# Optimization experiments

Measured on AMD Instinct MI355X. Metric: run time of the kernel, lower is better.

Reference implementation:

```python
import jax, jax.numpy as jnp
import numpy as np

N_NODES = 60000
IN_CH = 128
HID = 32
ACT_DIM = 6
N_EDGES = 600000


def setup_inputs() -> dict:
    key = jax.random.key(0)
    ks = jax.random.split(key, 10)
    state = jax.random.normal(ks[0], (N_NODES, IN_CH), dtype=jnp.float32)
    edge_index = jax.random.randint(ks[1], (2, N_EDGES), 0, N_NODES, dtype=jnp.int64)
    s_g = 1.0 / np.sqrt(IN_CH)
    s_h = 1.0 / np.sqrt(HID)
    Wg = jax.random.uniform(ks[2], (IN_CH, IN_CH), jnp.float32, -s_g, s_g)
    bg = jax.random.uniform(ks[3], (IN_CH,), jnp.float32, -s_g, s_g)
    W1 = jax.random.uniform(ks[4], (IN_CH, HID), jnp.float32, -s_g, s_g)
    b1 = jax.random.uniform(ks[5], (HID,), jnp.float32, -s_g, s_g)
    W2 = jax.random.uniform(ks[6], (HID, HID), jnp.float32, -s_h, s_h)
    b2 = jax.random.uniform(ks[7], (HID,), jnp.float32, -s_h, s_h)
    W3 = jax.random.uniform(ks[8], (HID, 1), jnp.float32, -s_h, s_h)
    b3 = jax.random.uniform(ks[9], (1,), jnp.float32, -s_h, s_h)
    return {"state": state, "Wg": Wg, "bg": bg, "W1": W1, "b1": b1,
            "W2": W2, "b2": b2, "W3": W3, "b3": b3, "edge_index": edge_index}


def reference(state, Wg, bg, W1, b1, W2, b2, W3, b3, edge_index):
    N = state.shape[0]
    # GCNConv: add self-loops, symmetric degree normalization
    loop = jnp.arange(N, dtype=edge_index.dtype)
    src = jnp.concatenate([edge_index[0], loop])
    dst = jnp.concatenate([edge_index[1], loop])
    deg = jax.ops.segment_sum(jnp.ones_like(dst, dtype=state.dtype), dst, num_segments=N)
    dinv = jax.lax.rsqrt(deg)  # deg >= 1 thanks to self-loops
    norm = dinv[src] * dinv[dst]  # [E+N]
    h = state @ Wg  # [N, C]
    agg = jax.ops.segment_sum(h[src] * norm[:, None], dst, num_segments=N) + bg
    out = jax.nn.relu(agg)
    x = (out + state).reshape(-1, ACT_DIM, IN_CH)  # [B, 6, C]
    x = jax.nn.leaky_relu(x @ W1 + b1)
    x = jax.nn.leaky_relu(x @ W2 + b2)
    conc = jax.nn.softplus(x @ W3 + b3)[..., 0]  # [B, 6]
    # deterministic, mode==0
    action = conc / (conc.sum() + 1e-20)
    return action
```

## Files before the change

kernel.cpp:

```cpp
#include <hip/hip_runtime.h>
#include <hip/hip_bf16.h>
#include <math.h>

#define N_NODES 60000
#define IN_CH   128
#define HID     32
#define N_EDGES 600000
#define CAP     48

#define WS_CNT    0
#define WS_SUM    60000
#define WS_BUCKET 60008
#define WS_HS     2940032
#define WS_X      10620032

typedef float  v4f __attribute__((ext_vector_type(4)));
typedef short  v8s __attribute__((ext_vector_type(8)));

static __device__ inline short f2bf(float f) {
    __hip_bfloat16 h = __float2bfloat16(f);
    union { __hip_bfloat16 h; short s; } u; u.h = h; return u.s;
}
static __device__ inline float bflo(unsigned int u) { return __uint_as_float(u << 16); }
static __device__ inline float bfhi(unsigned int u) { return __uint_as_float(u & 0xffff0000u); }

__launch_bounds__(256)
__global__ void k_fat(const float* __restrict__ state, const float* __restrict__ Wg,
                      const int* __restrict__ eidx, int* __restrict__ cnt,
                      int* __restrict__ bucket, unsigned short* __restrict__ hs) {
    __shared__ __align__(16) short Bs[128 * 136];
    const int bid = blockIdx.x;
    const int r7 = bid % 7, q7 = bid / 7;
    const int t = threadIdx.x;

    if (r7 >= 2) {
        const int hb = q7 * 5 + (r7 - 2);
        const int i = hb * 256 + t;
        if (i < N_EDGES) {
            int s = eidx[i];
            int d = eidx[N_EDGES + i];
            int slot = atomicAdd(&cnt[d], 1);
            if (slot < CAP) bucket[d * CAP + slot] = s;
        }
        return;
    }

    const int gb = q7 * 2 + r7;

    for (int idx = t; idx < 128 * 128; idx += 256) {
        int k = idx >> 7, n = idx & 127;
        Bs[n * 136 + k] = f2bf(Wg[idx]);
    }
    __syncthreads();

    const int w = t >> 6, lane = t & 63;
    const int quad = lane >> 4, m = lane & 15;
    const int rowBase = gb * 64;
    int arow = rowBase + w * 16 + m;
    if (arow > N_NODES - 1) arow = N_NODES - 1;

    v8s a[4];
    const float4* sp = (const float4*)(state + (size_t)arow * 128);
#pragma unroll
    for (int q = 0; q < 4; ++q) {
        float4 v0 = sp[q * 8 + quad * 2];
        float4 v1 = sp[q * 8 + quad * 2 + 1];
        v8s af;
        af[0] = f2bf(v0.x); af[1] = f2bf(v0.y); af[2] = f2bf(v0.z); af[3] = f2bf(v0.w);
        af[4] = f2bf(v1.x); af[5] = f2bf(v1.y); af[6] = f2bf(v1.z); af[7] = f2bf(v1.w);
        a[q] = af;
    }

    v4f acc[8];
#pragma unroll
    for (int tt = 0; tt < 8; ++tt) acc[tt] = (v4f)0.f;

#pragma unroll
    for (int tt = 0; tt < 8; ++tt) {
        const short* bp = &Bs[(tt * 16 + m) * 136];
#pragma unroll
        for (int q = 0; q < 4; ++q) {
            v8s b = *(const v8s*)(bp + q * 32 + quad * 8);
            acc[tt] = __builtin_amdgcn_mfma_f32_16x16x32_bf16(a[q], b, acc[tt], 0, 0, 0);
        }
    }

#pragma unroll
    for (int tt = 0; tt < 8; ++tt) {
#pragma unroll
        for (int r = 0; r < 4; ++r) {
            int rr = rowBase + w * 16 + quad * 4 + r;
            if (rr < N_NODES)
                hs[(size_t)rr * 128 + tt * 16 + m] = (unsigned short)f2bf(acc[tt][r]);
        }
    }
}

__launch_bounds__(256)
__global__ void k_gather(const unsigned short* __restrict__ hs, const float* __restrict__ state,
                         const int* __restrict__ cnt, const int* __restrict__ bucket,
                         const float* __restrict__ bg, unsigned int* __restrict__ xb) {
    const int wave = threadIdx.x >> 6, lane = threadIdx.x & 63;
    const int row = blockIdx.x * 4 + wave;
    if (row >= N_NODES) return;
    const int ci = cnt[row];
    const float dinv = rsqrtf((float)ci + 1.0f);
    const int nb = ci < CAP ? ci : CAP;

    int slot = 0; float dv = 0.f;
    if (lane < nb) {
        slot = bucket[row * CAP + lane];
        dv = rsqrtf((float)cnt[slot] + 1.0f);
    }

    const unsigned int* hp = (const unsigned int*)hs;
    float ax, ay;
    {
        unsigned int u = hp[(size_t)row * 64 + lane];
        ax = bflo(u) * dinv;
        ay = bfhi(u) * dinv;
    }
    int s = 0;
    for (; s + 8 <= nb; s += 8) {
        int s0 = __shfl(slot, s + 0, 64), s1 = __shfl(slot, s + 1, 64);
        int s2 = __shfl(slot, s + 2, 64), s3 = __shfl(slot, s + 3, 64);
        int s4 = __shfl(slot, s + 4, 64), s5 = __shfl(slot, s + 5, 64);
        int s6 = __shfl(slot, s + 6, 64), s7 = __shfl(slot, s + 7, 64);
        float d0 = __shfl(dv, s + 0, 64), d1 = __shfl(dv, s + 1, 64);
        float d2 = __shfl(dv, s + 2, 64), d3 = __shfl(dv, s + 3, 64);
        float d4 = __shfl(dv, s + 4, 64), d5 = __shfl(dv, s + 5, 64);
        float d6 = __shfl(dv, s + 6, 64), d7 = __shfl(dv, s + 7, 64);
        unsigned int u0 = hp[(size_t)s0 * 64 + lane];
        unsigned int u1 = hp[(size_t)s1 * 64 + lane];
        unsigned int u2 = hp[(size_t)s2 * 64 + lane];
        unsigned int u3 = hp[(size_t)s3 * 64 + lane];
        unsigned int u4 = hp[(size_t)s4 * 64 + lane];
        unsigned int u5 = hp[(size_t)s5 * 64 + lane];
        unsigned int u6 = hp[(size_t)s6 * 64 + lane];
        unsigned int u7 = hp[(size_t)s7 * 64 + lane];
        ax = fmaf(d0, bflo(u0), ax); ay = fmaf(d0, bfhi(u0), ay);
        ax = fmaf(d1, bflo(u1), ax); ay = fmaf(d1, bfhi(u1), ay);
        ax = fmaf(d2, bflo(u2), ax); ay = fmaf(d2, bfhi(u2), ay);
        ax = fmaf(d3, bflo(u3), ax); ay = fmaf(d3, bfhi(u3), ay);
        ax = fmaf(d4, bflo(u4), ax); ay = fmaf(d4, bfhi(u4), ay);
        ax = fmaf(d5, bflo(u5), ax); ay = fmaf(d5, bfhi(u5), ay);
        ax = fmaf(d6, bflo(u6), ax); ay = fmaf(d6, bfhi(u6), ay);
        ax = fmaf(d7, bflo(u7), ax); ay = fmaf(d7, bfhi(u7), ay);
    }
    for (; s + 4 <= nb; s += 4) {
        int s0 = __shfl(slot, s + 0, 64), s1 = __shfl(slot, s + 1, 64);
        int s2 = __shfl(slot, s + 2, 64), s3 = __shfl(slot, s + 3, 64);
        float d0 = __shfl(dv, s + 0, 64), d1 = __shfl(dv, s + 1, 64);
        float d2 = __shfl(dv, s + 2, 64), d3 = __shfl(dv, s + 3, 64);
        unsigned int u0 = hp[(size_t)s0 * 64 + lane];
        unsigned int u1 = hp[(size_t)s1 * 64 + lane];
        unsigned int u2 = hp[(size_t)s2 * 64 + lane];
        unsigned int u3 = hp[(size_t)s3 * 64 + lane];
        ax = fmaf(d0, bflo(u0), ax); ay = fmaf(d0, bfhi(u0), ay);
        ax = fmaf(d1, bflo(u1), ax); ay = fmaf(d1, bfhi(u1), ay);
        ax = fmaf(d2, bflo(u2), ax); ay = fmaf(d2, bfhi(u2), ay);
        ax = fmaf(d3, bflo(u3), ax); ay = fmaf(d3, bfhi(u3), ay);
    }
    for (; s < nb; ++s) {
        int s0 = __shfl(slot, s, 64);
        float d0 = __shfl(dv, s, 64);
        unsigned int u = hp[(size_t)s0 * 64 + lane];
        ax = fmaf(d0, bflo(u), ax);
        ay = fmaf(d0, bfhi(u), ay);
    }
    float2 bgv = ((const float2*)bg)[lane];
    float2 st  = ((const float2*)state)[(size_t)row * 64 + lane];
    float ox = fmaxf(fmaf(dinv, ax, bgv.x), 0.f) + st.x;
    float oy = fmaxf(fmaf(dinv, ay, bgv.y), 0.f) + st.y;
    unsigned int pack = ((unsigned int)(unsigned short)f2bf(oy) << 16)
                      | ((unsigned int)(unsigned short)f2bf(ox));
    xb[(size_t)row * 64 + lane] = pack;
}

__launch_bounds__(256)
__global__ void k_mlp(const unsigned int* __restrict__ xb,
                      const float* __restrict__ W1, const float* __restrict__ b1,
                      const float* __restrict__ W2, const float* __restrict__ b2,
                      const float* __restrict__ W3, const float* __restrict__ b3,
                      float* __restrict__ out, float* __restrict__ sum) {
    __shared__ float4 W1s[128 * 8];
    __shared__ float4 W2s[32 * 8];
    __shared__ float  W3s[32];
    __shared__ float  wred[4];
    const int t = threadIdx.x;
#pragma unroll
    for (int i = 0; i < 4; ++i) W1s[t + 256 * i] = ((const float4*)W1)[t + 256 * i];
    W2s[t] = ((const float4*)W2)[t];
    if (t < 32) W3s[t] = W3[t];
    __syncthreads();

    const int r = blockIdx.x * 256 + t;
    float sp = 0.f;
    if (r < N_NODES) {
        float h1[32];
#pragma unroll
        for (int j = 0; j < 32; ++j) h1[j] = b1[j];
        const v8s* xr = (const v8s*)(xb + (size_t)r * 64);
#pragma unroll 2
        for (int k8 = 0; k8 < 16; ++k8) {
            v8s xv = xr[k8];
#pragma unroll
            for (int jj = 0; jj < 8; ++jj) {
                float xk = __uint_as_float(((unsigned int)(unsigned short)xv[jj]) << 16);
                const int k = k8 * 8 + jj;
#pragma unroll
                for (int j4 = 0; j4 < 8; ++j4) {
                    float4 w = W1s[k * 8 + j4];
                    h1[j4 * 4 + 0] = fmaf(xk, w.x, h1[j4 * 4 + 0]);
                    h1[j4 * 4 + 1] = fmaf(xk, w.y, h1[j4 * 4 + 1]);
                    h1[j4 * 4 + 2] = fmaf(xk, w.z, h1[j4 * 4 + 2]);
                    h1[j4 * 4 + 3] = fmaf(xk, w.w, h1[j4 * 4 + 3]);
                }
            }
        }
        float z1[32];
#pragma unroll
        for (int j = 0; j < 32; ++j) z1[j] = h1[j] > 0.f ? h1[j] : 0.01f * h1[j];
        float h2[32];
#pragma unroll
        for (int j = 0; j < 32; ++j) h2[j] = b2[j];
#pragma unroll
        for (int k = 0; k < 32; ++k) {
            float zk = z1[k];
#pragma unroll
            for (int j4 = 0; j4 < 8; ++j4) {
                float4 w = W2s[k * 8 + j4];
                h2[j4 * 4 + 0] = fmaf(zk, w.x, h2[j4 * 4 + 0]);
                h2[j4 * 4 + 1] = fmaf(zk, w.y, h2[j4 * 4 + 1]);
                h2[j4 * 4 + 2] = fmaf(zk, w.z, h2[j4 * 4 + 2]);
                h2[j4 * 4 + 3] = fmaf(zk, w.w, h2[j4 * 4 + 3]);
            }
        }
        float a3 = b3[0];
#pragma unroll
        for (int j = 0; j < 32; ++j) {
            float z2 = h2[j] > 0.f ? h2[j] : 0.01f * h2[j];
            a3 = fmaf(z2, W3s[j], a3);
        }
        sp = fmaxf(a3, 0.f) + log1pf(expf(-fabsf(a3)));
        out[r] = sp;
    }
    float p = sp;
#pragma unroll
    for (int off = 32; off >= 1; off >>= 1) p += __shfl_xor(p, off, 64);
    if ((t & 63) == 0) wred[t >> 6] = p;
    __syncthreads();
    if (t == 0) atomicAdd(sum, (wred[0] + wred[1]) + (wred[2] + wred[3]));
}

__global__ void k_norm(const float* __restrict__ sum, float* __restrict__ out) {
    int i = blockIdx.x * blockDim.x + threadIdx.x;
    if (i < N_NODES / 4) {
        float inv = 1.0f / (*sum + 1e-20f);
        float4* o4 = (float4*)out;
        float4 v = o4[i];
        v.x *= inv; v.y *= inv; v.z *= inv; v.w *= inv;
        o4[i] = v;
    }
}

extern "C" void kernel_launch(void* const* d_in, const int* in_sizes, int n_in,
                              void* d_out, int out_size, void* d_ws, size_t ws_size,
                              hipStream_t stream) {
    const float* state = (const float*)d_in[0];
    const float* Wg    = (const float*)d_in[1];
    const float* bg    = (const float*)d_in[2];
    const float* W1    = (const float*)d_in[3];
    const float* b1    = (const float*)d_in[4];
    const float* W2    = (const float*)d_in[5];
    const float* b2    = (const float*)d_in[6];
    const float* W3    = (const float*)d_in[7];
    const float* b3    = (const float*)d_in[8];
    const int*   eidx  = (const int*)d_in[9];
    float* out = (float*)d_out;

    int*   wi = (int*)d_ws;
    float* wf = (float*)d_ws;
    int*   cnt    = wi + WS_CNT;
    float* sum    = wf + WS_SUM;
    int*   bucket = wi + WS_BUCKET;
    unsigned short* hs = (unsigned short*)(wf + WS_HS);
    unsigned int*   xb = (unsigned int*)(wf + WS_X);

    hipMemsetAsync(cnt, 0, 60001 * sizeof(int), stream);

    k_fat<<<3282, 256, 0, stream>>>(state, Wg, eidx, cnt, bucket, hs);
    k_gather<<<(N_NODES + 3) / 4, 256, 0, stream>>>(hs, state, cnt, bucket, bg, xb);
    k_mlp<<<(N_NODES + 255) / 256, 256, 0, stream>>>(xb, W1, b1, W2, b2, W3, b3, out, sum);
    k_norm<<<(N_NODES / 4 + 255) / 256, 256, 0, stream>>>(sum, out);
}
```

Before: 184.1 us.

## Coarsen GEMM and histogram blocks in fused kernel, vectorize edge loads

New measurement: 192.6 us. 1.05x slower.

```diff
diff --git a/kernel.cpp b/kernel.cpp
--- a/kernel.cpp
+++ b/kernel.cpp
@@ -23,6 +23,9 @@
 }
 static __device__ inline float bflo(unsigned int u) { return __uint_as_float(u << 16); }
 static __device__ inline float bfhi(unsigned int u) { return __uint_as_float(u & 0xffff0000u); }
+
+#define GEMM_BLOCKS 235
+#define HIST_BLOCKS 586
 
 __launch_bounds__(256)
 __global__ void k_fat(const float* __restrict__ state, const float* __restrict__ Wg,
@@ -30,22 +33,34 @@
                       int* __restrict__ bucket, unsigned short* __restrict__ hs) {
     __shared__ __align__(16) short Bs[128 * 136];
     const int bid = blockIdx.x;
-    const int r7 = bid % 7, q7 = bid / 7;
     const int t = threadIdx.x;
 
-    if (r7 >= 2) {
-        const int hb = q7 * 5 + (r7 - 2);
-        const int i = hb * 256 + t;
-        if (i < N_EDGES) {
-            int s = eidx[i];
-            int d = eidx[N_EDGES + i];
-            int slot = atomicAdd(&cnt[d], 1);
-            if (slot < CAP) bucket[d * CAP + slot] = s;
+    if (bid >= GEMM_BLOCKS) {
+        const int hb = bid - GEMM_BLOCKS;
+        const int i = hb * 1024 + t * 4;
+        if (i + 3 < N_EDGES) {
+            int4 s4 = *(const int4*)(eidx + i);
+            int4 d4 = *(const int4*)(eidx + N_EDGES + i);
+            int sl0 = atomicAdd(&cnt[d4.x], 1);
+            int sl1 = atomicAdd(&cnt[d4.y], 1);
+            int sl2 = atomicAdd(&cnt[d4.z], 1);
+            int sl3 = atomicAdd(&cnt[d4.w], 1);
+            if (sl0 < CAP) __builtin_nontemporal_store(s4.x, &bucket[d4.x * CAP + sl0]);
+            if (sl1 < CAP) __builtin_nontemporal_store(s4.y, &bucket[d4.y * CAP + sl1]);
+            if (sl2 < CAP) __builtin_nontemporal_store(s4.z, &bucket[d4.z * CAP + sl2]);
+            if (sl3 < CAP) __builtin_nontemporal_store(s4.w, &bucket[d4.w * CAP + sl3]);
+        } else {
+            for (int k = i; k < N_EDGES; ++k) {
+                int s = eidx[k];
+                int d = eidx[N_EDGES + k];
+                int slot = atomicAdd(&cnt[d], 1);
+                if (slot < CAP) __builtin_nontemporal_store(s, &bucket[d * CAP + slot]);
+            }
         }
         return;
     }
 
-    const int gb = q7 * 2 + r7;
+    const int gb = bid;
 
     for (int idx = t; idx < 128 * 128; idx += 256) {
         int k = idx >> 7, n = idx & 127;
@@ -55,43 +70,47 @@
 
     const int w = t >> 6, lane = t & 63;
     const int quad = lane >> 4, m = lane & 15;
-    const int rowBase = gb * 64;
-    int arow = rowBase + w * 16 + m;
-    if (arow > N_NODES - 1) arow = N_NODES - 1;
-
-    v8s a[4];
-    const float4* sp = (const float4*)(state + (size_t)arow * 128);
-#pragma unroll
-    for (int q = 0; q < 4; ++q) {
-        float4 v0 = sp[q * 8 + quad * 2];
-        float4 v1 = sp[q * 8 + quad * 2 + 1];
-        v8s af;
-        af[0] = f2bf(v0.x); af[1] = f2bf(v0.y); af[2] = f2bf(v0.z); af[3] = f2bf(v0.w);
-        af[4] = f2bf(v1.x); af[5] = f2bf(v1.y); af[6] = f2bf(v1.z); af[7] = f2bf(v1.w);
-        a[q] = af;
-    }
-
-    v4f acc[8];
-#pragma unroll
-    for (int tt = 0; tt < 8; ++tt) acc[tt] = (v4f)0.f;
-
-#pragma unroll
-    for (int tt = 0; tt < 8; ++tt) {
-        const short* bp = &Bs[(tt * 16 + m) * 136];
+
+#pragma unroll 1
+    for (int strip = 0; strip < 4; ++strip) {
+        const int rowBase = gb * 256 + strip * 64;
+        int arow = rowBase + w * 16 + m;
+        if (arow > N_NODES - 1) arow = N_NODES - 1;
+
+        v8s a[4];
+        const float4* sp = (const float4*)(state + (size_t)arow * 128);
 #pragma unroll
         for (int q = 0; q < 4; ++q) {
-            v8s b = *(const v8s*)(bp + q * 32 + quad * 8);
-            acc[tt] = __builtin_amdgcn_mfma_f32_16x16x32_bf16(a[q], b, acc[tt], 0, 0, 0);
-        }
-    }
-
-#pragma unroll
-    for (int tt = 0; tt < 8; ++tt) {
-#pragma unroll
-        for (int r = 0; r < 4; ++r) {
-            int rr = rowBase + w * 16 + quad * 4 + r;
-            if (rr < N_NODES)
-                hs[(size_t)rr * 128 + tt * 16 + m] = (unsigned short)f2bf(acc[tt][r]);
+            float4 v0 = sp[q * 8 + quad * 2];
+            float4 v1 = sp[q * 8 + quad * 2 + 1];
+            v8s af;
+            af[0] = f2bf(v0.x); af[1] = f2bf(v0.y); af[2] = f2bf(v0.z); af[3] = f2bf(v0.w);
+            af[4] = f2bf(v1.x); af[5] = f2bf(v1.y); af[6] = f2bf(v1.z); af[7] = f2bf(v1.w);
+            a[q] = af;
+        }
+
+        v4f acc[8];
+#pragma unroll
+        for (int tt = 0; tt < 8; ++tt) acc[tt] = (v4f)0.f;
+
+#pragma unroll
+        for (int tt = 0; tt < 8; ++tt) {
+            const short* bp = &Bs[(tt * 16 + m) * 136];
+#pragma unroll
+            for (int q = 0; q < 4; ++q) {
+                v8s b = *(const v8s*)(bp + q * 32 + quad * 8);
+                acc[tt] = __builtin_amdgcn_mfma_f32_16x16x32_bf16(a[q], b, acc[tt], 0, 0, 0);
+            }
+        }
+
+#pragma unroll
+        for (int tt = 0; tt < 8; ++tt) {
+#pragma unroll
+            for (int r = 0; r < 4; ++r) {
+                int rr = rowBase + w * 16 + quad * 4 + r;
+                if (rr < N_NODES)
+                    hs[(size_t)rr * 128 + tt * 16 + m] = (unsigned short)f2bf(acc[tt][r]);
+            }
         }
     }
 }
@@ -289,7 +308,7 @@
 
     hipMemsetAsync(cnt, 0, 60001 * sizeof(int), stream);
 
-    k_fat<<<3282, 256, 0, stream>>>(state, Wg, eidx, cnt, bucket, hs);
+    k_fat<<<GEMM_BLOCKS + HIST_BLOCKS, 256, 0, stream>>>(state, Wg, eidx, cnt, bucket, hs);
     k_gather<<<(N_NODES + 3) / 4, 256, 0, stream>>>(hs, state, cnt, bucket, bg, xb);
     k_mlp<<<(N_NODES + 255) / 256, 256, 0, stream>>>(xb, W1, b1, W2, b2, W3, b3, out, sum);
     k_norm<<<(N_NODES / 4 + 255) / 256, 256, 0, stream>>>(sum, out);
```
